# Kernel tuning notes

Hardware: AMD Instinct MI355X
Metric: run time of the kernel (lower is better)

Reference implementation:

```python
import jax, jax.numpy as jnp
import numpy as np

EOS = 1e-10
N = 6000          # nnodes
E = 192000        # n_edges (avg degree 32)
D_IN = 512        # input_dim
H = 128           # hidden_dim
ALPHA = 1.0
TEMP = 1.0
BIAS = 1e-4


def setup_inputs() -> dict:
    key = jax.random.key(0)
    k1, k2, k3, k4, k5, k6, k7 = jax.random.split(key, 7)
    features = jax.random.normal(k1, (N, D_IN), dtype=jnp.float32)
    edges = jax.random.randint(k2, (2, E), 0, N)
    # params: embedding Linear(D_IN->H) and edge MLP Linear(2H->1)
    w_emb = jax.random.normal(k3, (D_IN, H), dtype=jnp.float32) * 0.05
    b_emb = jnp.zeros((H,), jnp.float32)
    w_mlp = jax.random.normal(k4, (2 * H, 1), dtype=jnp.float32) * 0.05
    b_mlp = jnp.zeros((1,), jnp.float32)
    # gumbel-sigmoid noise: eps = (bias-(1-bias))*u + (1-bias)  in [bias, 1-bias]
    u = jax.random.uniform(k5, (E,), dtype=jnp.float32)
    eps = (BIAS - (1.0 - BIAS)) * u + (1.0 - BIAS)
    gate_noise = jnp.log(eps) - jnp.log(1.0 - eps)
    return {"features": features, "edges": edges, "w_emb": w_emb, "b_emb": b_emb,
            "w_mlp": w_mlp, "b_mlp": b_mlp, "gate_noise": gate_noise}


def _normalize_sym(adj):
    d = adj.sum(axis=1)
    inv = 1.0 / (jnp.sqrt(d) + EOS)
    return adj * inv[:, None] * inv[None, :]


def reference(features, edges, w_emb, b_emb, w_mlp, b_mlp, gate_noise):
    # node embeddings: single Linear + ReLU
    emb = jax.nn.relu(features @ w_emb + b_emb)              # [N, H]
    h0 = emb[edges[0]]                                       # [E, H]
    h1 = emb[edges[1]]                                       # [E, H]
    s1 = (jnp.concatenate([h0, h1], axis=1) @ w_mlp + b_mlp).ravel()
    s2 = (jnp.concatenate([h1, h0], axis=1) @ w_mlp + b_mlp).ravel()
    raw = (s1 + s2) * 0.5                                    # [E]
    # gumbel-sigmoid gating
    weights_lp = jax.nn.sigmoid((gate_noise + raw) / TEMP)
    weights_hp = 1.0 - weights_lp

    eye = jnp.eye(N, dtype=features.dtype)

    def build_adj(w):
        adj = jnp.zeros((N, N), features.dtype).at[edges[0], edges[1]].set(w)
        return _normalize_sym(adj + eye)

    adj_lp = build_adj(weights_lp)
    adj_hp = build_adj(weights_hp)
    mask = jnp.zeros((N, N), features.dtype).at[edges[0], edges[1]].set(1.0)
    adj_hp = eye - adj_hp * mask * ALPHA
    adj_unnorm = jnp.zeros((N, N), features.dtype).at[edges[0], edges[1]].set(1.0)
    return (adj_lp, adj_hp, weights_lp, weights_hp, adj_unnorm)
```

## Files before the change

### kernel.cpp

```cpp
#include <hip/hip_runtime.h>
#include <math.h>

#define NNODES 6000
#define NEDGES 192000
#define DIN 512
#define HDIM 128
#define ALPHA 1.0f
#define EOS 1e-10f
#define KMAX 256

static const size_t NN = (size_t)NNODES * (size_t)NNODES;

__global__ __launch_bounds__(128) void embed_g_kernel(
    const float* __restrict__ feat, const float* __restrict__ w_emb,
    const float* __restrict__ b_emb, const float* __restrict__ w_mlp,
    float* __restrict__ g) {
  __shared__ float sf[8 * DIN];
  __shared__ float red[2][8];
  const int t = threadIdx.x;
  const int nb = blockIdx.x * 8;

  const float4* f4 = (const float4*)(feat + (size_t)nb * DIN);
  float4* s4 = (float4*)sf;
#pragma unroll
  for (int k = 0; k < 8; ++k) s4[k * 128 + t] = f4[k * 128 + t];
  __syncthreads();

  const int h = t;
  float acc[8];
  const float b = b_emb[h];
#pragma unroll
  for (int n = 0; n < 8; ++n) acc[n] = b;

  const float4* sf4 = (const float4*)sf;
#pragma unroll 2
  for (int d4 = 0; d4 < DIN / 4; ++d4) {
    const float w0 = w_emb[(d4 * 4 + 0) * HDIM + h];
    const float w1 = w_emb[(d4 * 4 + 1) * HDIM + h];
    const float w2 = w_emb[(d4 * 4 + 2) * HDIM + h];
    const float w3 = w_emb[(d4 * 4 + 3) * HDIM + h];
#pragma unroll
    for (int n = 0; n < 8; ++n) {
      const float4 f = sf4[n * (DIN / 4) + d4];
      acc[n] += f.x * w0;
      acc[n] += f.y * w1;
      acc[n] += f.z * w2;
      acc[n] += f.w * w3;
    }
  }

  const float wv = 0.5f * (w_mlp[h] + w_mlp[HDIM + h]);
  const int lane = t & 63, wave = t >> 6;
#pragma unroll
  for (int n = 0; n < 8; ++n) {
    float v = fmaxf(acc[n], 0.0f) * wv;
    for (int off = 32; off > 0; off >>= 1) v += __shfl_down(v, off, 64);
    if (lane == 0) red[wave][n] = v;
  }
  __syncthreads();
  if (t < 8) g[nb + t] = red[0][t] + red[1][t];
}

__global__ __launch_bounds__(256) void edge_bucket_kernel(
    const int* __restrict__ edges, const float* __restrict__ g,
    const float* __restrict__ noise, const float* __restrict__ b_mlp,
    float* __restrict__ w_lp, float* __restrict__ w_hp,
    int* __restrict__ cnt, int* __restrict__ slots) {
  const int e = blockIdx.x * blockDim.x + threadIdx.x;
  if (e >= NEDGES) return;
  const int u = edges[e];
  const int v = edges[NEDGES + e];
  const float raw = g[u] + g[v] + b_mlp[0];
  const float x = noise[e] + raw;
  const float wl = 1.0f / (1.0f + expf(-x));
  w_lp[e] = wl;
  w_hp[e] = 1.0f - wl;
  const int k = atomicAdd(&cnt[u], 1);
  if (k < KMAX) slots[(size_t)u * NNODES + k] = e;
}

__global__ __launch_bounds__(256) void row_dedup_deg_kernel(
    const int* __restrict__ edges, const float* __restrict__ w_lp,
    const float* __restrict__ w_hp, const int* __restrict__ cnt,
    int* __restrict__ slots, float* __restrict__ deg_lp,
    float* __restrict__ deg_hp) {
  __shared__ int se[4][KMAX];
  __shared__ int sv[4][KMAX];
  __shared__ float sl[4][KMAX];
  __shared__ float sh[4][KMAX];
  const int wid = threadIdx.x >> 6;
  const int lane = threadIdx.x & 63;
  const int r = blockIdx.x * 4 + wid;

  int k = cnt[r];
  if (k > KMAX) k = KMAX;
  int* srow = slots + (size_t)r * NNODES;
  for (int i = lane; i < k; i += 64) {
    const int e = srow[i];
    se[wid][i] = e;
    sv[wid][i] = edges[NEDGES + e];
    sl[wid][i] = w_lp[e];
    sh[wid][i] = w_hp[e];
  }
  __syncthreads();

  float suml = 0.0f, sumh = 0.0f;
  for (int i = lane; i < k; i += 64) {
    const int e = se[wid][i];
    const int v = sv[wid][i];
    int win = 1;
    for (int j = 0; j < k; ++j) {
      if (sv[wid][j] == v && se[wid][j] > e) { win = 0; break; }
    }
    if (win) {
      suml += sl[wid][i];
      sumh += sh[wid][i];
    }
    srow[i] = (e << 14) | (v << 1) | win;
  }
  for (int off = 32; off > 0; off >>= 1) {
    suml += __shfl_down(suml, off, 64);
    sumh += __shfl_down(sumh, off, 64);
  }
  if (lane == 0) {
    deg_lp[r] = suml;
    deg_hp[r] = sumh;
  }
}

__global__ __launch_bounds__(256) void node_inv_kernel(
    const float* __restrict__ deg_lp, const float* __restrict__ deg_hp,
    float* __restrict__ inv_lp, float* __restrict__ inv_hp) {
  const int i = blockIdx.x * blockDim.x + threadIdx.x;
  if (i >= NNODES) return;
  inv_lp[i] = 1.0f / (sqrtf(deg_lp[i] + 1.0f) + EOS);
  inv_hp[i] = 1.0f / (sqrtf(deg_hp[i] + 1.0f) + EOS);
}

__global__ __launch_bounds__(256) void paint_kernel(
    const float* __restrict__ w_lp, const float* __restrict__ w_hp,
    const float* __restrict__ inv_lp, const float* __restrict__ inv_hp,
    const int* __restrict__ cnt, float* __restrict__ adj_lp,
    float* __restrict__ adj_hp, float* __restrict__ unnorm) {
  __shared__ int scol[KMAX];
  __shared__ float slp[KMAX];
  __shared__ float shp[KMAX];
  __shared__ int has_self;
  __shared__ float sdiag[2];

  const int t = threadIdx.x;
  const int r = blockIdx.x;
  int k = cnt[r];
  if (k > KMAX) k = KMAX;
  const float il = inv_lp[r];
  const float ih = inv_hp[r];

  float* lp_row = adj_lp + (size_t)r * NNODES;
  float* hp_row = adj_hp + (size_t)r * NNODES;
  float* un_row = unnorm + (size_t)r * NNODES;
  const int* srow = (const int*)un_row;

  if (t == 0) {
    has_self = 0;
    sdiag[0] = 0.0f;
    sdiag[1] = 0.0f;
  }
  __syncthreads();

  if (t < k) {
    const int raw = srow[t];
    const int win = raw & 1;
    const int v = (raw >> 1) & 0x1FFF;
    const int e = (int)(((unsigned)raw) >> 14);
    const float wl = w_lp[e];
    const float wh = w_hp[e];
    scol[t] = (v << 1) | win;
    slp[t] = wl * il * inv_lp[v];
    shp[t] = -ALPHA * wh * ih * inv_hp[v];
    if (v == r) {
      has_self = 1;
      if (win) {
        sdiag[0] = wl;
        sdiag[1] = wh;
      }
    }
  }
  __syncthreads();

  const float4 z = make_float4(0.0f, 0.0f, 0.0f, 0.0f);
  float4* lp4 = (float4*)lp_row;
  float4* hp4 = (float4*)hp_row;
  float4* un4 = (float4*)un_row;
  for (int c = t; c < NNODES / 4; c += 256) {
    lp4[c] = z;
    hp4[c] = z;
    un4[c] = z;
  }
  __syncthreads();

  if (t < k) {
    const int cw = scol[t];
    const int win = cw & 1;
    const int v = cw >> 1;
    un_row[v] = 1.0f;
    if (win && v != r) {
      lp_row[v] = slp[t];
      hp_row[v] = shp[t];
    }
  }
  if (t == 0) {
    if (has_self) {
      lp_row[r] = (sdiag[0] + 1.0f) * il * il;
      hp_row[r] = 1.0f - (sdiag[1] + 1.0f) * ih * ih * ALPHA;
    } else {
      lp_row[r] = il * il;
      hp_row[r] = 1.0f;
    }
  }
}

extern "C" void kernel_launch(void* const* d_in, const int* in_sizes, int n_in,
                              void* d_out, int out_size, void* d_ws,
                              size_t ws_size, hipStream_t stream) {
  const float* feat  = (const float*)d_in[0];
  const int*   edges = (const int*)d_in[1];
  const float* w_emb = (const float*)d_in[2];
  const float* b_emb = (const float*)d_in[3];
  const float* w_mlp = (const float*)d_in[4];
  const float* b_mlp = (const float*)d_in[5];
  const float* noise = (const float*)d_in[6];

  float* out    = (float*)d_out;
  float* adj_lp = out;
  float* adj_hp = out + NN;
  float* w_lp   = out + 2 * NN;
  float* w_hp   = w_lp + NEDGES;
  float* unnorm = w_hp + NEDGES;

  float* g      = (float*)d_ws;
  float* deg_lp = g + NNODES;
  float* deg_hp = deg_lp + NNODES;
  float* inv_lp = deg_hp + NNODES;
  float* inv_hp = inv_lp + NNODES;
  int*   cnt    = (int*)(inv_hp + NNODES);

  hipMemsetAsync(cnt, 0, NNODES * sizeof(int), stream);

  embed_g_kernel<<<NNODES / 8, 128, 0, stream>>>(feat, w_emb, b_emb, w_mlp, g);

  edge_bucket_kernel<<<NEDGES / 256, 256, 0, stream>>>(
      edges, g, noise, b_mlp, w_lp, w_hp, cnt, (int*)unnorm);

  row_dedup_deg_kernel<<<NNODES / 4, 256, 0, stream>>>(
      edges, w_lp, w_hp, cnt, (int*)unnorm, deg_lp, deg_hp);

  node_inv_kernel<<<(NNODES + 255) / 256, 256, 0, stream>>>(
      deg_lp, deg_hp, inv_lp, inv_hp);

  paint_kernel<<<NNODES, 256, 0, stream>>>(w_lp, w_hp, inv_lp, inv_hp, cnt,
                                           adj_lp, adj_hp, unnorm);
}
```

Baseline: 530.2 us.

## Assemble adjacency rows in shared-memory chunks and fold small kernels together

The paint kernel now builds each output row in 1000-column shared-memory chunks and writes each chunk once with non-temporal vector stores. Before, it zeroed the whole row in global memory and then scattered the nonzero values into it, so those cache lines were written twice. The memset of the counters moves into the embedding kernel and the inverse-degree computation moves into the dedup kernel, removing one memset and one launch. The sigmoid uses the fast __expf intrinsic, which may change results slightly, and the chunk loop adds several barriers per row.

```diff
diff --git a/kernel.cpp b/kernel.cpp
--- a/kernel.cpp
+++ b/kernel.cpp
@@ -8,17 +8,22 @@
 #define ALPHA 1.0f
 #define EOS 1e-10f
 #define KMAX 256
+#define CHUNK 1000
+
+typedef float f32x4 __attribute__((ext_vector_type(4)));
 
 static const size_t NN = (size_t)NNODES * (size_t)NNODES;
 
 __global__ __launch_bounds__(128) void embed_g_kernel(
     const float* __restrict__ feat, const float* __restrict__ w_emb,
     const float* __restrict__ b_emb, const float* __restrict__ w_mlp,
-    float* __restrict__ g) {
+    float* __restrict__ g, int* __restrict__ cnt) {
   __shared__ float sf[8 * DIN];
   __shared__ float red[2][8];
   const int t = threadIdx.x;
   const int nb = blockIdx.x * 8;
+
+  if (t < 8) cnt[nb + t] = 0;
 
   const float4* f4 = (const float4*)(feat + (size_t)nb * DIN);
   float4* s4 = (float4*)sf;
@@ -72,7 +77,7 @@
   const int v = edges[NEDGES + e];
   const float raw = g[u] + g[v] + b_mlp[0];
   const float x = noise[e] + raw;
-  const float wl = 1.0f / (1.0f + expf(-x));
+  const float wl = 1.0f / (1.0f + __expf(-x));
   w_lp[e] = wl;
   w_hp[e] = 1.0f - wl;
   const int k = atomicAdd(&cnt[u], 1);
@@ -82,8 +87,8 @@
 __global__ __launch_bounds__(256) void row_dedup_deg_kernel(
     const int* __restrict__ edges, const float* __restrict__ w_lp,
     const float* __restrict__ w_hp, const int* __restrict__ cnt,
-    int* __restrict__ slots, float* __restrict__ deg_lp,
-    float* __restrict__ deg_hp) {
+    int* __restrict__ slots, float* __restrict__ inv_lp,
+    float* __restrict__ inv_hp) {
   __shared__ int se[4][KMAX];
   __shared__ int sv[4][KMAX];
   __shared__ float sl[4][KMAX];
@@ -123,18 +128,9 @@
     sumh += __shfl_down(sumh, off, 64);
   }
   if (lane == 0) {
-    deg_lp[r] = suml;
-    deg_hp[r] = sumh;
-  }
-}
-
-__global__ __launch_bounds__(256) void node_inv_kernel(
-    const float* __restrict__ deg_lp, const float* __restrict__ deg_hp,
-    float* __restrict__ inv_lp, float* __restrict__ inv_hp) {
-  const int i = blockIdx.x * blockDim.x + threadIdx.x;
-  if (i >= NNODES) return;
-  inv_lp[i] = 1.0f / (sqrtf(deg_lp[i] + 1.0f) + EOS);
-  inv_hp[i] = 1.0f / (sqrtf(deg_hp[i] + 1.0f) + EOS);
+    inv_lp[r] = 1.0f / (sqrtf(suml + 1.0f) + EOS);
+    inv_hp[r] = 1.0f / (sqrtf(sumh + 1.0f) + EOS);
+  }
 }
 
 __global__ __launch_bounds__(256) void paint_kernel(
@@ -142,11 +138,14 @@
     const float* __restrict__ inv_lp, const float* __restrict__ inv_hp,
     const int* __restrict__ cnt, float* __restrict__ adj_lp,
     float* __restrict__ adj_hp, float* __restrict__ unnorm) {
-  __shared__ int scol[KMAX];
-  __shared__ float slp[KMAX];
-  __shared__ float shp[KMAX];
-  __shared__ int has_self;
-  __shared__ float sdiag[2];
+  __shared__ __align__(16) float chl[CHUNK];
+  __shared__ __align__(16) float chh[CHUNK];
+  __shared__ __align__(16) float chu[CHUNK];
+  __shared__ int colw[KMAX + 1];
+  __shared__ float vlp[KMAX + 1];
+  __shared__ float vhp[KMAX + 1];
+  __shared__ int colu[KMAX];
+  __shared__ int skk, shas;
 
   const int t = threadIdx.x;
   const int r = blockIdx.x;
@@ -160,11 +159,7 @@
   float* un_row = unnorm + (size_t)r * NNODES;
   const int* srow = (const int*)un_row;
 
-  if (t == 0) {
-    has_self = 0;
-    sdiag[0] = 0.0f;
-    sdiag[1] = 0.0f;
-  }
+  if (t == 0) shas = 0;
   __syncthreads();
 
   if (t < k) {
@@ -174,48 +169,70 @@
     const int e = (int)(((unsigned)raw) >> 14);
     const float wl = w_lp[e];
     const float wh = w_hp[e];
-    scol[t] = (v << 1) | win;
-    slp[t] = wl * il * inv_lp[v];
-    shp[t] = -ALPHA * wh * ih * inv_hp[v];
-    if (v == r) {
-      has_self = 1;
-      if (win) {
-        sdiag[0] = wl;
-        sdiag[1] = wh;
+    colu[t] = v;
+    if (v == r) shas = 1;
+    if (win) {
+      if (v == r) {
+        colw[t] = r;
+        vlp[t] = (wl + 1.0f) * il * il;
+        vhp[t] = 1.0f - (wh + 1.0f) * ih * ih * ALPHA;
+      } else {
+        colw[t] = v;
+        vlp[t] = wl * il * inv_lp[v];
+        vhp[t] = -ALPHA * wh * ih * inv_hp[v];
       }
-    }
-  }
-  __syncthreads();
-
-  const float4 z = make_float4(0.0f, 0.0f, 0.0f, 0.0f);
-  float4* lp4 = (float4*)lp_row;
-  float4* hp4 = (float4*)hp_row;
-  float4* un4 = (float4*)un_row;
-  for (int c = t; c < NNODES / 4; c += 256) {
-    lp4[c] = z;
-    hp4[c] = z;
-    un4[c] = z;
-  }
-  __syncthreads();
-
-  if (t < k) {
-    const int cw = scol[t];
-    const int win = cw & 1;
-    const int v = cw >> 1;
-    un_row[v] = 1.0f;
-    if (win && v != r) {
-      lp_row[v] = slp[t];
-      hp_row[v] = shp[t];
-    }
-  }
+    } else {
+      colw[t] = -1;
+    }
+  }
+  __syncthreads();
+
   if (t == 0) {
-    if (has_self) {
-      lp_row[r] = (sdiag[0] + 1.0f) * il * il;
-      hp_row[r] = 1.0f - (sdiag[1] + 1.0f) * ih * ih * ALPHA;
+    if (!shas) {
+      colw[k] = r;
+      vlp[k] = il * il;
+      vhp[k] = 1.0f;
+      skk = k + 1;
     } else {
-      lp_row[r] = il * il;
-      hp_row[r] = 1.0f;
-    }
+      skk = k;
+    }
+  }
+  __syncthreads();
+  const int kk = skk;
+
+  const f32x4 z = {0.0f, 0.0f, 0.0f, 0.0f};
+  f32x4* chl4 = (f32x4*)chl;
+  f32x4* chh4 = (f32x4*)chh;
+  f32x4* chu4 = (f32x4*)chu;
+
+  for (int c0 = 0; c0 < NNODES; c0 += CHUNK) {
+    if (t < CHUNK / 4) {
+      chl4[t] = z;
+      chh4[t] = z;
+      chu4[t] = z;
+    }
+    __syncthreads();
+    for (int j = t; j < kk; j += 256) {
+      const int d = colw[j] - c0;
+      if ((unsigned)d < (unsigned)CHUNK) {
+        chl[d] = vlp[j];
+        chh[d] = vhp[j];
+      }
+    }
+    for (int j = t; j < k; j += 256) {
+      const int d = colu[j] - c0;
+      if ((unsigned)d < (unsigned)CHUNK) chu[d] = 1.0f;
+    }
+    __syncthreads();
+    if (t < CHUNK / 4) {
+      const f32x4 L = chl4[t];
+      const f32x4 H = chh4[t];
+      const f32x4 U = chu4[t];
+      __builtin_nontemporal_store(L, (f32x4*)(lp_row + c0) + t);
+      __builtin_nontemporal_store(H, (f32x4*)(hp_row + c0) + t);
+      __builtin_nontemporal_store(U, (f32x4*)(un_row + c0) + t);
+    }
+    __syncthreads();
   }
 }
 
@@ -238,24 +255,18 @@
   float* unnorm = w_hp + NEDGES;
 
   float* g      = (float*)d_ws;
-  float* deg_lp = g + NNODES;
-  float* deg_hp = deg_lp + NNODES;
-  float* inv_lp = deg_hp + NNODES;
+  float* inv_lp = g + NNODES;
   float* inv_hp = inv_lp + NNODES;
   int*   cnt    = (int*)(inv_hp + NNODES);
 
-  hipMemsetAsync(cnt, 0, NNODES * sizeof(int), stream);
-
-  embed_g_kernel<<<NNODES / 8, 128, 0, stream>>>(feat, w_emb, b_emb, w_mlp, g);
+  embed_g_kernel<<<NNODES / 8, 128, 0, stream>>>(feat, w_emb, b_emb, w_mlp, g,
+                                                 cnt);
 
   edge_bucket_kernel<<<NEDGES / 256, 256, 0, stream>>>(
       edges, g, noise, b_mlp, w_lp, w_hp, cnt, (int*)unnorm);
 
   row_dedup_deg_kernel<<<NNODES / 4, 256, 0, stream>>>(
-      edges, w_lp, w_hp, cnt, (int*)unnorm, deg_lp, deg_hp);
-
-  node_inv_kernel<<<(NNODES + 255) / 256, 256, 0, stream>>>(
-      deg_lp, deg_hp, inv_lp, inv_hp);
+      edges, w_lp, w_hp, cnt, (int*)unnorm, inv_lp, inv_hp);
 
   paint_kernel<<<NNODES, 256, 0, stream>>>(w_lp, w_hp, inv_lp, inv_hp, cnt,
                                            adj_lp, adj_hp, unnorm);
```

Result: no change. 530.3 us (+0.0%).
